# Kernel optimization log

Hardware: AMD Instinct MI355X
Metric: run time of the kernel (lower is better)

Reference implementation:

```python
import jax, jax.numpy as jnp
import numpy as np

ALPHA = 1.0
BETTA = 1.0
WEIGHT_ROTE = 0.5
WEIGHT_MSE = 0.5
EPS_MASK = 1e-8

B, D = 16384, 768


def setup_inputs() -> dict:
    key = jax.random.key(0)
    k1, k2, k3, k4 = jax.random.split(key, 4)
    return {
        "init_img_vec": jax.random.normal(k1, (B, 1, D), dtype=jnp.float32),
        "next_img_vec": jax.random.normal(k2, (B, 1, D), dtype=jnp.float32),
        "init_unclip": jax.random.normal(k3, (B, 1, D), dtype=jnp.float32),
        "pred_unclip": jax.random.normal(k4, (B, 1, D), dtype=jnp.float32),
    }


def _transform_loss(init_img_vec, next_img_vec, init_unclip, pred_unclip):
    diff_img = (init_img_vec - next_img_vec)[:, 0, :].astype(jnp.float32)      # [B, D]
    diff_unclip = init_unclip[:, 0, :].astype(jnp.float32) - pred_unclip[:, 0, :]

    # mask-compaction: rows with ||diff_img|| > 1e-8 are kept. We keep the full
    # batch (jit-safe) and weight the batch-mean by the mask; identical result.
    norm1 = jnp.linalg.norm(diff_img, axis=-1, keepdims=True)                  # [B, 1]
    mask = (norm1 > EPS_MASK)                                                  # [B, 1]
    mask_f = mask.astype(jnp.float32)
    cnt = jnp.maximum(jnp.sum(mask_f), 1.0)

    v1 = jnp.where(mask, diff_img, 1.0)   # safe values on masked-out rows
    v2 = diff_unclip

    # RotationVectors.angle / unit_vector
    n1 = v1 / jnp.linalg.norm(v1, axis=-1, keepdims=True)                      # [B, D]
    norm2 = jnp.linalg.norm(v2, axis=-1, keepdims=True)
    cos_ang = jnp.clip(jnp.sum(v1 * v2, axis=-1, keepdims=True)
                       / (jnp.linalg.norm(v1, axis=-1, keepdims=True) * norm2),
                       -1.0, 1.0)
    a = jnp.arccos(cos_ang)                                                    # [B, 1]

    w = v2 - n1 * jnp.sum(n1 * v2, axis=-1, keepdims=True)
    n2 = w / jnp.linalg.norm(w, axis=-1, keepdims=True)                        # [B, D]

    sin_a = jnp.sin(a)                 # [B, 1]
    cos_a_m1 = jnp.cos(a) - 1.0        # [B, 1]

    # transform = alpha*sin_a*(n2 n1^T - n1 n2^T) + betta*(cos_a-1)*(n1 n1^T + n2 n2^T)
    # u_transform = transform @ ones ; (M v^T) @ 1 = M * sum(v), so no DxD needed.
    s1 = jnp.sum(n1, axis=-1, keepdims=True)   # n1 . u
    s2 = jnp.sum(n2, axis=-1, keepdims=True)   # n2 . u
    u_transform = (ALPHA * sin_a * (n2 * s1 - n1 * s2)
                   + BETTA * cos_a_m1 * (n1 * s1 + n2 * s2))                   # [B, D]

    # loss_u: MSE(u_transform, 0), mean over masked rows -> [D]
    loss_u = jnp.sum((u_transform ** 2) * mask_f, axis=0) / cnt
    # loss_I: MSE(I @ ones, ones) = 0 exactly -> [D]
    loss_I = jnp.zeros((diff_img.shape[-1],), dtype=jnp.float32)

    loss_u = jnp.nan_to_num(loss_u, nan=0.0, posinf=0.1, neginf=-0.1)
    loss_I = jnp.nan_to_num(loss_I, nan=0.0, posinf=0.1, neginf=-0.1)

    # plain MSE over the FULL (unmasked) batch, mean over dim 0 -> [D]
    mse = jnp.mean((diff_img - diff_unclip) ** 2, axis=0) + loss_I

    return WEIGHT_ROTE * loss_u, WEIGHT_MSE * mse


def reference(init_img_vec, next_img_vec, init_unclip, pred_unclip):
    return _transform_loss(init_img_vec, next_img_vec, init_unclip, pred_unclip)
```

## Files before the change

kernel.cpp:

```cpp
#include <hip/hip_runtime.h>
#include <math.h>


constexpr int D      = 768;
constexpr int B_ROWS = 16384;
constexpr int BDIM   = 512;
constexpr int NBLK   = 1024;
constexpr int WPB    = BDIM / 64;
constexpr int RPW    = B_ROWS / (NBLK * WPB);
constexpr int RG     = 64;
constexpr int NRG    = NBLK / RG;

constexpr size_t CNT_OFF = (size_t)NBLK * 2 * D;
constexpr size_t P2_OFF  = CNT_OFF + NBLK;

__global__ void zero_ws_kernel(float* __restrict__ ws, int n) {
    int i = blockIdx.x * blockDim.x + threadIdx.x;
    if (i < n) ws[i] = 0.0f;
}

template <bool PARTIALS>
__global__ __launch_bounds__(BDIM)
void transform_loss_main(const float* __restrict__ g_init_img,
                         const float* __restrict__ g_next_img,
                         const float* __restrict__ g_init_unclip,
                         const float* __restrict__ g_pred_unclip,
                         float* __restrict__ ws)
{
    const int lane  = threadIdx.x & 63;
    const int wave  = threadIdx.x >> 6;
    const int gwave = blockIdx.x * WPB + wave;

    float acc_u[12], acc_m[12];
#pragma unroll
    for (int i = 0; i < 12; ++i) { acc_u[i] = 0.f; acc_m[i] = 0.f; }
    float local_cnt = 0.f;

#pragma unroll
    for (int r = 0; r < RPW; ++r) {
        const int row = gwave * RPW + r;
        const size_t base = (size_t)row * D + (size_t)(lane * 4);

        float4 va[3], vb[3], vc[3], vd[3];
#pragma unroll
        for (int t = 0; t < 3; ++t) {
            va[t] = *(const float4*)(g_init_img    + base + t * 256);
            vb[t] = *(const float4*)(g_next_img    + base + t * 256);
            vc[t] = *(const float4*)(g_init_unclip + base + t * 256);
            vd[t] = *(const float4*)(g_pred_unclip + base + t * 256);
        }

        float d1[12], d2[12];
        float sA = 0.f, sC = 0.f, sAB = 0.f, sS1 = 0.f, sS2 = 0.f;
#pragma unroll
        for (int t = 0; t < 3; ++t) {
            const float a4[4] = {va[t].x, va[t].y, va[t].z, va[t].w};
            const float b4[4] = {vb[t].x, vb[t].y, vb[t].z, vb[t].w};
            const float c4[4] = {vc[t].x, vc[t].y, vc[t].z, vc[t].w};
            const float e4[4] = {vd[t].x, vd[t].y, vd[t].z, vd[t].w};
#pragma unroll
            for (int j = 0; j < 4; ++j) {
                float x = a4[j] - b4[j];
                float y = c4[j] - e4[j];
                d1[t * 4 + j] = x; d2[t * 4 + j] = y;
                sA  = fmaf(x, x, sA);
                sC  = fmaf(y, y, sC);
                sAB = fmaf(x, y, sAB);
                sS1 += x;
                sS2 += y;
            }
        }
#pragma unroll
        for (int m = 1; m < 64; m <<= 1) {
            sA  += __shfl_xor(sA,  m);
            sC  += __shfl_xor(sC,  m);
            sAB += __shfl_xor(sAB, m);
            sS1 += __shfl_xor(sS1, m);
            sS2 += __shfl_xor(sS2, m);
        }
#pragma unroll
        for (int i = 0; i < 12; ++i) {
            float dd = d1[i] - d2[i];
            acc_m[i] = fmaf(dd, dd, acc_m[i]);
        }
        if (sA > 1e-16f) {
            local_cnt += 1.f;
            float nA  = sqrtf(sA);
            float rA  = 1.f / nA;
            float nC  = sqrtf(sC);
            float cosang = sAB / (nA * nC);
            cosang = fminf(fmaxf(cosang, -1.f), 1.f);
            float sin_a = sqrtf(fmaxf(1.f - cosang * cosang, 0.f));
            float cm1 = cosang - 1.f;
            float k  = sAB / sA;
            float W  = sC - sAB * k;
            float rW = 1.f / sqrtf(W);
            float s1 = sS1 * rA;
            float s2 = (sS2 - sS1 * k) * rW;
            float p  = cm1 * s1 - sin_a * s2;
            float q  = sin_a * s1 + cm1 * s2;
            float c1 = p * rA - q * k * rW;
            float c2 = q * rW;
#pragma unroll
            for (int i = 0; i < 12; ++i) {
                float u = fmaf(d1[i], c1, d2[i] * c2);
                acc_u[i] = fmaf(u, u, acc_u[i]);
            }
        }
    }

    __shared__ float sh[2 * D];
    __shared__ float shcnt;
    if (threadIdx.x == 0) shcnt = 0.f;
    for (int i = threadIdx.x; i < 2 * D; i += BDIM) sh[i] = 0.f;
    __syncthreads();
#pragma unroll
    for (int t = 0; t < 3; ++t)
#pragma unroll
        for (int j = 0; j < 4; ++j) {
            int dIdx = t * 256 + lane * 4 + j;
            atomicAdd(&sh[dIdx],     acc_u[t * 4 + j]);
            atomicAdd(&sh[D + dIdx], acc_m[t * 4 + j]);
        }
    if (lane == 0) atomicAdd(&shcnt, local_cnt);
    __syncthreads();

    if (PARTIALS) {
        float* pb = ws + (size_t)blockIdx.x * (2 * D);
        for (int i = threadIdx.x; i < 2 * D; i += BDIM) pb[i] = sh[i];
        if (threadIdx.x == 0) ws[CNT_OFF + blockIdx.x] = shcnt;
    } else {
        for (int i = threadIdx.x; i < 2 * D; i += BDIM) atomicAdd(&ws[i], sh[i]);
        if (threadIdx.x == 0) atomicAdd(&ws[2 * D], shcnt);
    }
}

__global__ __launch_bounds__(BDIM)
void reduce_partials(const float* __restrict__ ws_in, float* __restrict__ ws_out)
{
    const int c  = blockIdx.x * BDIM + threadIdx.x;
    const int rg = blockIdx.y;
    if (c >= 2 * D) return;
    const float* p = ws_in + (size_t)rg * RG * (2 * D) + c;
    float s0 = 0.f, s1 = 0.f, s2 = 0.f, s3 = 0.f;
#pragma unroll 4
    for (int r = 0; r < RG; r += 4) {
        s0 += p[(size_t)(r + 0) * (2 * D)];
        s1 += p[(size_t)(r + 1) * (2 * D)];
        s2 += p[(size_t)(r + 2) * (2 * D)];
        s3 += p[(size_t)(r + 3) * (2 * D)];
    }
    ws_out[P2_OFF + (size_t)rg * (2 * D) + c] = (s0 + s1) + (s2 + s3);
}

__global__ __launch_bounds__(BDIM)
void finalize_tree(const float* __restrict__ ws, float* __restrict__ out)
{
    const int i = blockIdx.x * BDIM + threadIdx.x;
    float c = 0.f;
    for (int r = threadIdx.x; r < NBLK; r += BDIM) c += ws[CNT_OFF + r];
#pragma unroll
    for (int m = 1; m < 64; m <<= 1) c += __shfl_xor(c, m);
    __shared__ float sc[WPB];
    if ((threadIdx.x & 63) == 0) sc[threadIdx.x >> 6] = c;
    __syncthreads();
    float csum = 0.f;
#pragma unroll
    for (int wv = 0; wv < WPB; ++wv) csum += sc[wv];
    float cnt = fmaxf(csum, 1.f);

    if (i >= 2 * D) return;
    float s = 0.f;
#pragma unroll
    for (int g = 0; g < NRG; ++g) s += ws[P2_OFF + (size_t)g * (2 * D) + i];

    if (i < D) {
        float lu = s / cnt;
        if (isnan(lu)) lu = 0.f;
        else if (isinf(lu)) lu = (lu > 0.f) ? 0.1f : -0.1f;
        out[i] = 0.5f * lu;
    } else {
        out[i] = 0.5f * (s * (1.f / 16384.f));
    }
}

__global__ __launch_bounds__(BDIM)
void finalize_atomic(const float* __restrict__ ws, float* __restrict__ out)
{
    const int i = blockIdx.x * BDIM + threadIdx.x;
    if (i >= 2 * D) return;
    float cnt = fmaxf(ws[2 * D], 1.f);
    float s = ws[i];
    if (i < D) {
        float lu = s / cnt;
        if (isnan(lu)) lu = 0.f;
        else if (isinf(lu)) lu = (lu > 0.f) ? 0.1f : -0.1f;
        out[i] = 0.5f * lu;
    } else {
        out[i] = 0.5f * (s * (1.f / 16384.f));
    }
}

extern "C" void kernel_launch(void* const* d_in, const int* in_sizes, int n_in,
                              void* d_out, int out_size, void* d_ws, size_t ws_size,
                              hipStream_t stream) {
    const float* init_img    = (const float*)d_in[0];
    const float* next_img    = (const float*)d_in[1];
    const float* init_unclip = (const float*)d_in[2];
    const float* pred_unclip = (const float*)d_in[3];
    float* ws  = (float*)d_ws;
    float* out = (float*)d_out;

    const size_t need = (P2_OFF + (size_t)NRG * 2 * D) * sizeof(float);
    if (ws_size >= need) {
        transform_loss_main<true><<<NBLK, BDIM, 0, stream>>>(
            init_img, next_img, init_unclip, pred_unclip, ws);
        reduce_partials<<<dim3((2 * D + BDIM - 1) / BDIM, NRG), BDIM, 0, stream>>>(ws, ws);
        finalize_tree<<<(2 * D + BDIM - 1) / BDIM, BDIM, 0, stream>>>(ws, out);
    } else {
        zero_ws_kernel<<<(2 * D + 1 + BDIM - 1) / BDIM, BDIM, 0, stream>>>(ws, 2 * D + 1);
        transform_loss_main<false><<<NBLK, BDIM, 0, stream>>>(
            init_img, next_img, init_unclip, pred_unclip, ws);
        finalize_atomic<<<(2 * D + BDIM - 1) / BDIM, BDIM, 0, stream>>>(ws, out);
    }
}
```

Measured before the change: 251.2 us.

## Map one row per block with per-thread columns, removing shared-memory atomic reduction

```diff
diff --git a/kernel.cpp b/kernel.cpp
--- a/kernel.cpp
+++ b/kernel.cpp
@@ -4,10 +4,11 @@
 
 constexpr int D      = 768;
 constexpr int B_ROWS = 16384;
-constexpr int BDIM   = 512;
+constexpr int BDIM   = 384;
+constexpr int WPB    = BDIM / 64;
 constexpr int NBLK   = 1024;
-constexpr int WPB    = BDIM / 64;
-constexpr int RPW    = B_ROWS / (NBLK * WPB);
+constexpr int RPB    = B_ROWS / NBLK;
+constexpr int BDIM_R = 256;
 constexpr int RG     = 64;
 constexpr int NRG    = NBLK / RG;
 
@@ -21,124 +22,111 @@
 
 template <bool PARTIALS>
 __global__ __launch_bounds__(BDIM)
-void transform_loss_main(const float* __restrict__ g_init_img,
-                         const float* __restrict__ g_next_img,
-                         const float* __restrict__ g_init_unclip,
-                         const float* __restrict__ g_pred_unclip,
+void transform_loss_main(const float* __restrict__ gA,
+                         const float* __restrict__ gB,
+                         const float* __restrict__ gC,
+                         const float* __restrict__ gE,
                          float* __restrict__ ws)
 {
-    const int lane  = threadIdx.x & 63;
-    const int wave  = threadIdx.x >> 6;
-    const int gwave = blockIdx.x * WPB + wave;
-
-    float acc_u[12], acc_m[12];
-#pragma unroll
-    for (int i = 0; i < 12; ++i) { acc_u[i] = 0.f; acc_m[i] = 0.f; }
-    float local_cnt = 0.f;
-
-#pragma unroll
-    for (int r = 0; r < RPW; ++r) {
-        const int row = gwave * RPW + r;
-        const size_t base = (size_t)row * D + (size_t)(lane * 4);
-
-        float4 va[3], vb[3], vc[3], vd[3];
-#pragma unroll
-        for (int t = 0; t < 3; ++t) {
-            va[t] = *(const float4*)(g_init_img    + base + t * 256);
-            vb[t] = *(const float4*)(g_next_img    + base + t * 256);
-            vc[t] = *(const float4*)(g_init_unclip + base + t * 256);
-            vd[t] = *(const float4*)(g_pred_unclip + base + t * 256);
-        }
-
-        float d1[12], d2[12];
+    const int t    = threadIdx.x;
+    const int lane = t & 63;
+    const int wave = t >> 6;
+
+    float au0 = 0.f, au1 = 0.f, am0 = 0.f, am1 = 0.f, lcnt = 0.f;
+
+    __shared__ float red[2][WPB][8];
+
+    size_t base = (size_t)blockIdx.x * RPB * D + (size_t)(2 * t);
+    float2 va = *(const float2*)(gA + base);
+    float2 vb = *(const float2*)(gB + base);
+    float2 vc = *(const float2*)(gC + base);
+    float2 ve = *(const float2*)(gE + base);
+
+#pragma unroll
+    for (int r = 0; r < RPB; ++r) {
+        const float d1x = va.x - vb.x, d1y = va.y - vb.y;
+        const float d2x = vc.x - ve.x, d2y = vc.y - ve.y;
+        if (r + 1 < RPB) {
+            base += D;
+            va = *(const float2*)(gA + base);
+            vb = *(const float2*)(gB + base);
+            vc = *(const float2*)(gC + base);
+            ve = *(const float2*)(gE + base);
+        }
+        float pA  = fmaf(d1x, d1x, d1y * d1y);
+        float pC  = fmaf(d2x, d2x, d2y * d2y);
+        float pAB = fmaf(d1x, d2x, d1y * d2y);
+        float pS1 = d1x + d1y;
+        float pS2 = d2x + d2y;
+#pragma unroll
+        for (int m = 1; m < 64; m <<= 1) {
+            pA  += __shfl_xor(pA,  m);
+            pC  += __shfl_xor(pC,  m);
+            pAB += __shfl_xor(pAB, m);
+            pS1 += __shfl_xor(pS1, m);
+            pS2 += __shfl_xor(pS2, m);
+        }
+        if (lane == 0) {
+            red[r & 1][wave][0] = pA;
+            red[r & 1][wave][1] = pC;
+            red[r & 1][wave][2] = pAB;
+            red[r & 1][wave][3] = pS1;
+            red[r & 1][wave][4] = pS2;
+        }
+        __syncthreads();
         float sA = 0.f, sC = 0.f, sAB = 0.f, sS1 = 0.f, sS2 = 0.f;
 #pragma unroll
-        for (int t = 0; t < 3; ++t) {
-            const float a4[4] = {va[t].x, va[t].y, va[t].z, va[t].w};
-            const float b4[4] = {vb[t].x, vb[t].y, vb[t].z, vb[t].w};
-            const float c4[4] = {vc[t].x, vc[t].y, vc[t].z, vc[t].w};
-            const float e4[4] = {vd[t].x, vd[t].y, vd[t].z, vd[t].w};
-#pragma unroll
-            for (int j = 0; j < 4; ++j) {
-                float x = a4[j] - b4[j];
-                float y = c4[j] - e4[j];
-                d1[t * 4 + j] = x; d2[t * 4 + j] = y;
-                sA  = fmaf(x, x, sA);
-                sC  = fmaf(y, y, sC);
-                sAB = fmaf(x, y, sAB);
-                sS1 += x;
-                sS2 += y;
-            }
-        }
-#pragma unroll
-        for (int m = 1; m < 64; m <<= 1) {
-            sA  += __shfl_xor(sA,  m);
-            sC  += __shfl_xor(sC,  m);
-            sAB += __shfl_xor(sAB, m);
-            sS1 += __shfl_xor(sS1, m);
-            sS2 += __shfl_xor(sS2, m);
-        }
-#pragma unroll
-        for (int i = 0; i < 12; ++i) {
-            float dd = d1[i] - d2[i];
-            acc_m[i] = fmaf(dd, dd, acc_m[i]);
-        }
+        for (int w = 0; w < WPB; ++w) {
+            const float4 q = *(const float4*)&red[r & 1][w][0];
+            sA  += q.x; sC += q.y; sAB += q.z; sS1 += q.w;
+            sS2 += red[r & 1][w][4];
+        }
+        const float mdx = d1x - d2x, mdy = d1y - d2y;
+        am0 = fmaf(mdx, mdx, am0);
+        am1 = fmaf(mdy, mdy, am1);
         if (sA > 1e-16f) {
-            local_cnt += 1.f;
-            float nA  = sqrtf(sA);
-            float rA  = 1.f / nA;
-            float nC  = sqrtf(sC);
+            lcnt += 1.f;
+            const float nA  = sqrtf(sA);
+            const float rA  = 1.f / nA;
+            const float nC  = sqrtf(sC);
             float cosang = sAB / (nA * nC);
             cosang = fminf(fmaxf(cosang, -1.f), 1.f);
-            float sin_a = sqrtf(fmaxf(1.f - cosang * cosang, 0.f));
-            float cm1 = cosang - 1.f;
-            float k  = sAB / sA;
-            float W  = sC - sAB * k;
-            float rW = 1.f / sqrtf(W);
-            float s1 = sS1 * rA;
-            float s2 = (sS2 - sS1 * k) * rW;
-            float p  = cm1 * s1 - sin_a * s2;
-            float q  = sin_a * s1 + cm1 * s2;
-            float c1 = p * rA - q * k * rW;
-            float c2 = q * rW;
-#pragma unroll
-            for (int i = 0; i < 12; ++i) {
-                float u = fmaf(d1[i], c1, d2[i] * c2);
-                acc_u[i] = fmaf(u, u, acc_u[i]);
-            }
-        }
-    }
-
-    __shared__ float sh[2 * D];
-    __shared__ float shcnt;
-    if (threadIdx.x == 0) shcnt = 0.f;
-    for (int i = threadIdx.x; i < 2 * D; i += BDIM) sh[i] = 0.f;
-    __syncthreads();
-#pragma unroll
-    for (int t = 0; t < 3; ++t)
-#pragma unroll
-        for (int j = 0; j < 4; ++j) {
-            int dIdx = t * 256 + lane * 4 + j;
-            atomicAdd(&sh[dIdx],     acc_u[t * 4 + j]);
-            atomicAdd(&sh[D + dIdx], acc_m[t * 4 + j]);
-        }
-    if (lane == 0) atomicAdd(&shcnt, local_cnt);
-    __syncthreads();
+            const float sin_a = sqrtf(fmaxf(1.f - cosang * cosang, 0.f));
+            const float cm1 = cosang - 1.f;
+            const float k   = sAB / sA;
+            const float W   = sC - sAB * k;
+            const float rW  = 1.f / sqrtf(W);
+            const float s1  = sS1 * rA;
+            const float s2  = (sS2 - sS1 * k) * rW;
+            const float p   = cm1 * s1 - sin_a * s2;
+            const float q   = sin_a * s1 + cm1 * s2;
+            const float c1  = p * rA - q * k * rW;
+            const float c2  = q * rW;
+            const float ux = fmaf(d1x, c1, d2x * c2);
+            const float uy = fmaf(d1y, c1, d2y * c2);
+            au0 = fmaf(ux, ux, au0);
+            au1 = fmaf(uy, uy, au1);
+        }
+    }
 
     if (PARTIALS) {
         float* pb = ws + (size_t)blockIdx.x * (2 * D);
-        for (int i = threadIdx.x; i < 2 * D; i += BDIM) pb[i] = sh[i];
-        if (threadIdx.x == 0) ws[CNT_OFF + blockIdx.x] = shcnt;
-    } else {
-        for (int i = threadIdx.x; i < 2 * D; i += BDIM) atomicAdd(&ws[i], sh[i]);
-        if (threadIdx.x == 0) atomicAdd(&ws[2 * D], shcnt);
-    }
-}
-
-__global__ __launch_bounds__(BDIM)
+        *(float2*)(pb + 2 * t)     = make_float2(au0, au1);
+        *(float2*)(pb + D + 2 * t) = make_float2(am0, am1);
+        if (t == 0) ws[CNT_OFF + blockIdx.x] = lcnt;
+    } else {
+        atomicAdd(&ws[2 * t],         au0);
+        atomicAdd(&ws[2 * t + 1],     au1);
+        atomicAdd(&ws[D + 2 * t],     am0);
+        atomicAdd(&ws[D + 2 * t + 1], am1);
+        if (t == 0) atomicAdd(&ws[2 * D], lcnt);
+    }
+}
+
+__global__ __launch_bounds__(BDIM_R)
 void reduce_partials(const float* __restrict__ ws_in, float* __restrict__ ws_out)
 {
-    const int c  = blockIdx.x * BDIM + threadIdx.x;
+    const int c  = blockIdx.x * BDIM_R + threadIdx.x;
     const int rg = blockIdx.y;
     if (c >= 2 * D) return;
     const float* p = ws_in + (size_t)rg * RG * (2 * D) + c;
@@ -153,21 +141,21 @@
     ws_out[P2_OFF + (size_t)rg * (2 * D) + c] = (s0 + s1) + (s2 + s3);
 }
 
-__global__ __launch_bounds__(BDIM)
+__global__ __launch_bounds__(BDIM_R)
 void finalize_tree(const float* __restrict__ ws, float* __restrict__ out)
 {
-    const int i = blockIdx.x * BDIM + threadIdx.x;
+    const int i = blockIdx.x * BDIM_R + threadIdx.x;
     float c = 0.f;
-    for (int r = threadIdx.x; r < NBLK; r += BDIM) c += ws[CNT_OFF + r];
+    for (int r = threadIdx.x; r < NBLK; r += BDIM_R) c += ws[CNT_OFF + r];
 #pragma unroll
     for (int m = 1; m < 64; m <<= 1) c += __shfl_xor(c, m);
-    __shared__ float sc[WPB];
+    __shared__ float sc[BDIM_R / 64];
     if ((threadIdx.x & 63) == 0) sc[threadIdx.x >> 6] = c;
     __syncthreads();
     float csum = 0.f;
 #pragma unroll
-    for (int wv = 0; wv < WPB; ++wv) csum += sc[wv];
-    float cnt = fmaxf(csum, 1.f);
+    for (int wv = 0; wv < BDIM_R / 64; ++wv) csum += sc[wv];
+    const float cnt = fmaxf(csum, 1.f);
 
     if (i >= 2 * D) return;
     float s = 0.f;
@@ -184,13 +172,13 @@
     }
 }
 
-__global__ __launch_bounds__(BDIM)
+__global__ __launch_bounds__(BDIM_R)
 void finalize_atomic(const float* __restrict__ ws, float* __restrict__ out)
 {
-    const int i = blockIdx.x * BDIM + threadIdx.x;
+    const int i = blockIdx.x * BDIM_R + threadIdx.x;
     if (i >= 2 * D) return;
-    float cnt = fmaxf(ws[2 * D], 1.f);
-    float s = ws[i];
+    const float cnt = fmaxf(ws[2 * D], 1.f);
+    const float s = ws[i];
     if (i < D) {
         float lu = s / cnt;
         if (isnan(lu)) lu = 0.f;
@@ -215,12 +203,12 @@
     if (ws_size >= need) {
         transform_loss_main<true><<<NBLK, BDIM, 0, stream>>>(
             init_img, next_img, init_unclip, pred_unclip, ws);
-        reduce_partials<<<dim3((2 * D + BDIM - 1) / BDIM, NRG), BDIM, 0, stream>>>(ws, ws);
-        finalize_tree<<<(2 * D + BDIM - 1) / BDIM, BDIM, 0, stream>>>(ws, out);
-    } else {
-        zero_ws_kernel<<<(2 * D + 1 + BDIM - 1) / BDIM, BDIM, 0, stream>>>(ws, 2 * D + 1);
+        reduce_partials<<<dim3((2 * D + BDIM_R - 1) / BDIM_R, NRG), BDIM_R, 0, stream>>>(ws, ws);
+        finalize_tree<<<(2 * D + BDIM_R - 1) / BDIM_R, BDIM_R, 0, stream>>>(ws, out);
+    } else {
+        zero_ws_kernel<<<(2 * D + 1 + BDIM_R - 1) / BDIM_R, BDIM_R, 0, stream>>>(ws, 2 * D + 1);
         transform_loss_main<false><<<NBLK, BDIM, 0, stream>>>(
             init_img, next_img, init_unclip, pred_unclip, ws);
-        finalize_atomic<<<(2 * D + BDIM - 1) / BDIM, BDIM, 0, stream>>>(ws, out);
-    }
-}
+        finalize_atomic<<<(2 * D + BDIM_R - 1) / BDIM_R, BDIM_R, 0, stream>>>(ws, out);
+    }
+}
```

After: 219.2 us. -12.8%, faster.
